# Optimization experiments

Hardware: AMD Instinct MI355X
Metric: run time of the kernel (lower is better)

Reference implementation:

```python
import jax, jax.numpy as jnp
import numpy as np

B, S, IN, OUT = 4, 2048, 4096, 11008


def setup_inputs() -> dict:
    key = jax.random.key(0)
    k1, k2, k3, k4, k5 = jax.random.split(key, 5)
    x = jax.random.normal(k1, (B, S, IN), dtype=jnp.float32)
    # int8 quantized weights, stored as int32 per harness spec but values in int8 range
    W_int8 = jax.random.randint(k2, (OUT, IN), -128, 128, dtype=jnp.int32)
    # per-output-channel scales (small positive) and zero-points
    scale = jax.random.uniform(k3, (OUT,), dtype=jnp.float32, minval=1e-3, maxval=2e-2)
    zero = jax.random.uniform(k4, (OUT,), dtype=jnp.float32, minval=-8.0, maxval=8.0)
    bias = jax.random.normal(k5, (OUT,), dtype=jnp.float32) * 0.01
    return {"x": x, "W_int8": W_int8, "scale": scale, "zero": zero, "bias": bias}


def reference(x, W_int8, scale, zero, bias):
    # Original torch forward raises on NaN/Inf in x; for valid inputs the math is
    # quant_matmul: dequantize W = (W_int8 - zero) * scale (per output channel),
    # then y = x @ W.T + bias.
    W = (W_int8.astype(jnp.float32) - zero[:, None]) * scale[:, None]  # [OUT, IN]
    y = jnp.einsum('bsi,oi->bso', x, W) + bias  # [B, S, OUT]
    return y
```

## Files before the change

### kernel.cpp

```cpp
#include <hip/hip_runtime.h>
#include <stdint.h>


#define M_DIM 8192
#define N_DIM 11008
#define K_DIM 4096
#define NT    (K_DIM / 64)
#define BUFB  24576

typedef __attribute__((ext_vector_type(4))) int i32x4;


__global__ void convert_w_kernel(const int* __restrict__ w,
                                 int8_t* __restrict__ o, int n4) {
  int idx = blockIdx.x * blockDim.x + threadIdx.x;
  int stride = gridDim.x * blockDim.x;
  for (int i = idx; i < n4; i += stride) {
    int4 v = ((const int4*)w)[i];
    int r = (v.x & 255) | ((v.y & 255) << 8) | ((v.z & 255) << 16) | ((v.w & 255) << 24);
    ((int*)o)[i] = r;
  }
}

__global__ __launch_bounds__(256) void quantx_kernel(
    const float* __restrict__ x, int8_t* __restrict__ h8, int8_t* __restrict__ l8,
    float* __restrict__ xs, float* __restrict__ rsum) {
  const int row = blockIdx.x;
  const int t = threadIdx.x;
  const float4* px = (const float4*)(x + (size_t)row * K_DIM);
  float4 v[4];
  float mx = 0.f, sm = 0.f;
  #pragma unroll
  for (int i = 0; i < 4; ++i) {
    v[i] = px[i * 256 + t];
    mx = fmaxf(mx, fmaxf(fmaxf(fabsf(v[i].x), fabsf(v[i].y)),
                         fmaxf(fabsf(v[i].z), fabsf(v[i].w))));
    sm += v[i].x + v[i].y + v[i].z + v[i].w;
  }
  #pragma unroll
  for (int off = 32; off > 0; off >>= 1) {
    mx = fmaxf(mx, __shfl_down(mx, off));
    sm += __shfl_down(sm, off);
  }
  __shared__ float rmx[4], rsm[4];
  const int wv = t >> 6, ln = t & 63;
  if (ln == 0) { rmx[wv] = mx; rsm[wv] = sm; }
  __syncthreads();
  const float rowmax = fmaxf(fmaxf(rmx[0], rmx[1]), fmaxf(rmx[2], rmx[3]));
  if (t == 0) {
    xs[row] = rowmax > 0.f ? rowmax / 16256.f : 0.f;
    rsum[row] = rsm[0] + rsm[1] + rsm[2] + rsm[3];
  }
  const float inv = rowmax > 0.f ? 16256.f / rowmax : 0.f;
  int* hp = (int*)(h8 + (size_t)row * K_DIM);
  int* lp = (int*)(l8 + (size_t)row * K_DIM);
  #pragma unroll
  for (int i = 0; i < 4; ++i) {
    int q0 = (int)rintf(v[i].x * inv);
    int q1 = (int)rintf(v[i].y * inv);
    int q2 = (int)rintf(v[i].z * inv);
    int q3 = (int)rintf(v[i].w * inv);
    int h0 = (q0 + 64) >> 7, h1 = (q1 + 64) >> 7, h2 = (q2 + 64) >> 7, h3 = (q3 + 64) >> 7;
    int l0 = q0 - (h0 << 7), l1 = q1 - (h1 << 7), l2 = q2 - (h2 << 7), l3 = q3 - (h3 << 7);
    hp[i * 256 + t] = (h0 & 255) | ((h1 & 255) << 8) | ((h2 & 255) << 16) | ((h3 & 255) << 24);
    lp[i * 256 + t] = (l0 & 255) | ((l1 & 255) << 8) | ((l2 & 255) << 16) | ((l3 & 255) << 24);
  }
}


__device__ __forceinline__ void stage_tile(
    const int8_t* __restrict__ Ah, const int8_t* __restrict__ Al,
    const int8_t* __restrict__ Bw, size_t a_base, size_t b_base,
    int ks, int srow, int scol, int wave, int8_t* buf) {
  #pragma unroll
  for (int p = 0; p < 2; ++p) {
    const int8_t* g = Ah + a_base + (size_t)(p * 64 + srow) * K_DIM + ks + scol;
    __builtin_amdgcn_global_load_lds((const __attribute__((address_space(1))) void*)g,
        (__attribute__((address_space(3))) void*)(buf + p * 4096 + wave * 1024), 16, 0, 0);
  }
  #pragma unroll
  for (int p = 0; p < 2; ++p) {
    const int8_t* g = Al + a_base + (size_t)(p * 64 + srow) * K_DIM + ks + scol;
    __builtin_amdgcn_global_load_lds((const __attribute__((address_space(1))) void*)g,
        (__attribute__((address_space(3))) void*)(buf + 8192 + p * 4096 + wave * 1024), 16, 0, 0);
  }
  #pragma unroll
  for (int p = 0; p < 2; ++p) {
    const int8_t* g = Bw + b_base + (size_t)(p * 64 + srow) * K_DIM + ks + scol;
    __builtin_amdgcn_global_load_lds((const __attribute__((address_space(1))) void*)g,
        (__attribute__((address_space(3))) void*)(buf + 16384 + p * 4096 + wave * 1024), 16, 0, 0);
  }
}

__global__ __launch_bounds__(256, 2) void qgemm_kernel(
    const int8_t* __restrict__ Ah, const int8_t* __restrict__ Al,
    const int8_t* __restrict__ Bw, const float* __restrict__ xs,
    const float* __restrict__ rowsum, const float* __restrict__ scale,
    const float* __restrict__ zero, const float* __restrict__ bias,
    float* __restrict__ out) {
  __shared__ int8_t smem[2 * BUFB];

  const int tid = threadIdx.x;
  const int wave = tid >> 6;
  const int lane = tid & 63;

  const int bid = blockIdx.x;
  const int wg = (bid & 7) * 688 + (bid >> 3);
  const int group = wg / 688;
  const int rem = wg % 688;
  const int bm = group * 8 + (rem & 7);
  const int bn = rem >> 3;

  const int wr = wave >> 1;
  const int wc = wave & 1;

  i32x4 acch[4][4], accl[4][4];
  #pragma unroll
  for (int i = 0; i < 4; ++i)
    #pragma unroll
    for (int j = 0; j < 4; ++j) {
      acch[i][j] = (i32x4){0, 0, 0, 0};
      accl[i][j] = (i32x4){0, 0, 0, 0};
    }

  const int srow = tid >> 2;
  const int scol = ((((tid & 3) - ((tid >> 3) & 3)) & 3) << 4);
  const size_t a_base = (size_t)(bm * 128) * K_DIM;
  const size_t b_base = (size_t)(bn * 128) * K_DIM;

  const int fr = lane & 15;
  const int g = lane >> 4;
  const int scA = (((g + (fr >> 1)) & 3) << 4);

  int arow[4], brow[4];
  #pragma unroll
  for (int i = 0; i < 4; ++i) {
    arow[i] = (wr * 64 + i * 16 + fr) * 64 + scA;
    brow[i] = (wc * 64 + i * 16 + fr) * 64 + scA;
  }

  stage_tile(Ah, Al, Bw, a_base, b_base, 0, srow, scol, wave, smem);
  asm volatile("s_waitcnt vmcnt(0)" ::: "memory");
  __builtin_amdgcn_s_barrier();

  #pragma unroll 1
  for (int t = 0; t < NT; ++t) {
    const int8_t* buf = smem + (t & 1) * BUFB;
    int8_t* nxt = smem + ((t + 1) & 1) * BUFB;
    const int8_t* ldsAh_ = buf;
    const int8_t* ldsAl_ = buf + 8192;
    const int8_t* ldsB_  = buf + 16384;

    if (t + 1 < NT)
      stage_tile(Ah, Al, Bw, a_base, b_base, (t + 1) * 64, srow, scol, wave, nxt);

    i32x4 af[4][2], bf[4];
    #pragma unroll
    for (int ni = 0; ni < 4; ++ni)
      bf[ni] = *(const i32x4*)(ldsB_ + brow[ni]);
    #pragma unroll
    for (int mi = 0; mi < 4; ++mi) {
      af[mi][0] = *(const i32x4*)(ldsAh_ + arow[mi]);
      af[mi][1] = *(const i32x4*)(ldsAl_ + arow[mi]);
    }

    __builtin_amdgcn_s_setprio(1);
    #pragma unroll
    for (int mi = 0; mi < 4; ++mi)
      #pragma unroll
      for (int ni = 0; ni < 4; ++ni) {
        acch[mi][ni] = __builtin_amdgcn_mfma_i32_16x16x64_i8(af[mi][0], bf[ni], acch[mi][ni], 0, 0, 0);
        accl[mi][ni] = __builtin_amdgcn_mfma_i32_16x16x64_i8(af[mi][1], bf[ni], accl[mi][ni], 0, 0, 0);
      }
    __builtin_amdgcn_s_setprio(0);

    asm volatile("s_waitcnt lgkmcnt(0)" ::: "memory");
    asm volatile("s_waitcnt vmcnt(0)" ::: "memory");
    __builtin_amdgcn_s_barrier();
  }

  const int row0 = bm * 128 + wr * 64;
  const int col0 = bn * 128 + wc * 64;
  float s_[4], sz_[4], b_[4];
  #pragma unroll
  for (int ni = 0; ni < 4; ++ni) {
    const int n = col0 + ni * 16 + fr;
    const float s = scale[n];
    s_[ni] = s;
    sz_[ni] = s * zero[n];
    b_[ni] = bias[n];
  }
  #pragma unroll
  for (int mi = 0; mi < 4; ++mi) {
    #pragma unroll
    for (int j = 0; j < 4; ++j) {
      const int m = row0 + mi * 16 + g * 4 + j;
      const float xsm = xs[m];
      const float rs = rowsum[m];
      float* po = out + (size_t)m * N_DIM + col0;
      #pragma unroll
      for (int ni = 0; ni < 4; ++ni) {
        const float G = xsm * (128.f * (float)acch[mi][ni][j] + (float)accl[mi][ni][j]);
        po[ni * 16 + fr] = s_[ni] * G - sz_[ni] * rs + b_[ni];
      }
    }
  }
}


__global__ void fallback_kernel(const float* __restrict__ x, const int* __restrict__ w,
                                const float* __restrict__ scale, const float* __restrict__ zero,
                                const float* __restrict__ bias, float* __restrict__ out) {
  const int n = blockIdx.x * 16 + (threadIdx.x & 15);
  const int m = blockIdx.y * 16 + (threadIdx.x >> 4);
  const float z = zero[n];
  const float* xr = x + (size_t)m * K_DIM;
  const int* wr = w + (size_t)n * K_DIM;
  float acc = 0.f;
  for (int k = 0; k < K_DIM; ++k) acc += xr[k] * ((float)wr[k] - z);
  out[(size_t)m * N_DIM + n] = scale[n] * acc + bias[n];
}


extern "C" void kernel_launch(void* const* d_in, const int* in_sizes, int n_in,
                              void* d_out, int out_size, void* d_ws, size_t ws_size,
                              hipStream_t stream) {
  const float* x     = (const float*)d_in[0];
  const int*   w     = (const int*)d_in[1];
  const float* scale = (const float*)d_in[2];
  const float* zero  = (const float*)d_in[3];
  const float* bias  = (const float*)d_in[4];
  float* out = (float*)d_out;

  const size_t n_x = (size_t)M_DIM * K_DIM;
  const size_t n_w = (size_t)N_DIM * K_DIM;
  const size_t need = n_x * 2 + n_w + (size_t)M_DIM * 8;

  if (ws_size < need) {
    dim3 gr(N_DIM / 16, M_DIM / 16);
    fallback_kernel<<<gr, 256, 0, stream>>>(x, w, scale, zero, bias, out);
    return;
  }

  int8_t* x_h = (int8_t*)d_ws;
  int8_t* x_l = x_h + n_x;
  int8_t* w_8 = x_l + n_x;
  float* rsum = (float*)(w_8 + n_w);
  float* xs   = rsum + M_DIM;

  convert_w_kernel<<<2048, 256, 0, stream>>>(w, w_8, (int)(n_w / 4));
  quantx_kernel<<<M_DIM, 256, 0, stream>>>(x, x_h, x_l, xs, rsum);

  const int nblocks = (M_DIM / 128) * (N_DIM / 128);
  qgemm_kernel<<<nblocks, 256, 0, stream>>>(x_h, x_l, w_8, xs, rsum,
                                            scale, zero, bias, out);
}
```

Baseline: 824.8 us.

## Widen GEMM tile to 128x256 with 8 waves and 4-stage LDS pipeline

```diff
diff --git a/kernel.cpp b/kernel.cpp
--- a/kernel.cpp
+++ b/kernel.cpp
@@ -5,8 +5,8 @@
 #define M_DIM 8192
 #define N_DIM 11008
 #define K_DIM 4096
-#define NT    (K_DIM / 64)
-#define BUFB  24576
+#define NH    (K_DIM / 64)
+#define BUFH  32768
 
 typedef __attribute__((ext_vector_type(4))) int i32x4;
 
@@ -68,51 +68,87 @@
 }
 
 
-__device__ __forceinline__ void stage_tile(
+__device__ __forceinline__ void stage_half(
     const int8_t* __restrict__ Ah, const int8_t* __restrict__ Al,
     const int8_t* __restrict__ Bw, size_t a_base, size_t b_base,
-    int ks, int srow, int scol, int wave, int8_t* buf) {
+    int h, int trow, int scol, int wave, int8_t* smem) {
+  int8_t* buf = smem + (h & 3) * BUFH;
+  const int ks = h * 64;
+  {
+    const int8_t* g = Ah + a_base + (size_t)trow * K_DIM + ks + scol;
+    __builtin_amdgcn_global_load_lds((const __attribute__((address_space(1))) void*)g,
+        (__attribute__((address_space(3))) void*)(buf + wave * 1024), 16, 0, 0);
+  }
+  {
+    const int8_t* g = Al + a_base + (size_t)trow * K_DIM + ks + scol;
+    __builtin_amdgcn_global_load_lds((const __attribute__((address_space(1))) void*)g,
+        (__attribute__((address_space(3))) void*)(buf + 8192 + wave * 1024), 16, 0, 0);
+  }
   #pragma unroll
   for (int p = 0; p < 2; ++p) {
-    const int8_t* g = Ah + a_base + (size_t)(p * 64 + srow) * K_DIM + ks + scol;
+    const int8_t* g = Bw + b_base + (size_t)(p * 128 + trow) * K_DIM + ks + scol;
     __builtin_amdgcn_global_load_lds((const __attribute__((address_space(1))) void*)g,
-        (__attribute__((address_space(3))) void*)(buf + p * 4096 + wave * 1024), 16, 0, 0);
-  }
-  #pragma unroll
-  for (int p = 0; p < 2; ++p) {
-    const int8_t* g = Al + a_base + (size_t)(p * 64 + srow) * K_DIM + ks + scol;
-    __builtin_amdgcn_global_load_lds((const __attribute__((address_space(1))) void*)g,
-        (__attribute__((address_space(3))) void*)(buf + 8192 + p * 4096 + wave * 1024), 16, 0, 0);
-  }
-  #pragma unroll
-  for (int p = 0; p < 2; ++p) {
-    const int8_t* g = Bw + b_base + (size_t)(p * 64 + srow) * K_DIM + ks + scol;
-    __builtin_amdgcn_global_load_lds((const __attribute__((address_space(1))) void*)g,
-        (__attribute__((address_space(3))) void*)(buf + 16384 + p * 4096 + wave * 1024), 16, 0, 0);
-  }
-}
-
-__global__ __launch_bounds__(256, 2) void qgemm_kernel(
+        (__attribute__((address_space(3))) void*)(buf + 16384 + p * 8192 + wave * 1024), 16, 0, 0);
+  }
+}
+
+__device__ __forceinline__ i32x4 mfma_i8(i32x4 a, i32x4 b, i32x4 c) {
+  return __builtin_amdgcn_mfma_i32_16x16x64_i8(a, b, c, 0, 0, 0);
+}
+
+__device__ __forceinline__ void compute_half(
+    const int8_t* __restrict__ buf, const int* arow, const int* brow,
+    i32x4 (&acch)[4][4], i32x4 (&accl)[4][4]) {
+  const int8_t* pAh = buf;
+  const int8_t* pAl = buf + 8192;
+  const int8_t* pB  = buf + 16384;
+  i32x4 bf[4];
+  #pragma unroll
+  for (int ni = 0; ni < 4; ++ni) bf[ni] = *(const i32x4*)(pB + brow[ni]);
+  i32x4 cah = *(const i32x4*)(pAh + arow[0]);
+  i32x4 cal = *(const i32x4*)(pAl + arow[0]);
+  #pragma unroll
+  for (int mi = 0; mi < 4; ++mi) {
+    i32x4 nah = cah, nal = cal;
+    if (mi < 3) {
+      nah = *(const i32x4*)(pAh + arow[mi + 1]);
+      nal = *(const i32x4*)(pAl + arow[mi + 1]);
+    }
+    __builtin_amdgcn_s_setprio(1);
+    #pragma unroll
+    for (int ni = 0; ni < 4; ++ni)
+      acch[mi][ni] = mfma_i8(cah, bf[ni], acch[mi][ni]);
+    #pragma unroll
+    for (int ni = 0; ni < 4; ++ni)
+      accl[mi][ni] = mfma_i8(cal, bf[ni], accl[mi][ni]);
+    __builtin_amdgcn_s_setprio(0);
+    cah = nah; cal = nal;
+  }
+}
+
+#define VMW(n) asm volatile("s_waitcnt vmcnt(" #n ")" ::: "memory")
+
+__global__ __launch_bounds__(512, 2) void qgemm_kernel(
     const int8_t* __restrict__ Ah, const int8_t* __restrict__ Al,
     const int8_t* __restrict__ Bw, const float* __restrict__ xs,
     const float* __restrict__ rowsum, const float* __restrict__ scale,
     const float* __restrict__ zero, const float* __restrict__ bias,
     float* __restrict__ out) {
-  __shared__ int8_t smem[2 * BUFB];
+  extern __shared__ int8_t smem[];
 
   const int tid = threadIdx.x;
   const int wave = tid >> 6;
   const int lane = tid & 63;
 
   const int bid = blockIdx.x;
-  const int wg = (bid & 7) * 688 + (bid >> 3);
-  const int group = wg / 688;
-  const int rem = wg % 688;
+  const int wg = (bid & 7) * 344 + (bid >> 3);
+  const int group = wg / 344;
+  const int rem = wg % 344;
   const int bm = group * 8 + (rem & 7);
   const int bn = rem >> 3;
 
-  const int wr = wave >> 1;
-  const int wc = wave & 1;
+  const int wr = wave >> 2;
+  const int wc = wave & 3;
 
   i32x4 acch[4][4], accl[4][4];
   #pragma unroll
@@ -123,10 +159,10 @@
       accl[i][j] = (i32x4){0, 0, 0, 0};
     }
 
-  const int srow = tid >> 2;
+  const int trow = tid >> 2;
   const int scol = ((((tid & 3) - ((tid >> 3) & 3)) & 3) << 4);
   const size_t a_base = (size_t)(bm * 128) * K_DIM;
-  const size_t b_base = (size_t)(bn * 128) * K_DIM;
+  const size_t b_base = (size_t)((size_t)bn * 256) * K_DIM;
 
   const int fr = lane & 15;
   const int g = lane >> 4;
@@ -139,48 +175,32 @@
     brow[i] = (wc * 64 + i * 16 + fr) * 64 + scA;
   }
 
-  stage_tile(Ah, Al, Bw, a_base, b_base, 0, srow, scol, wave, smem);
-  asm volatile("s_waitcnt vmcnt(0)" ::: "memory");
-  __builtin_amdgcn_s_barrier();
+  stage_half(Ah, Al, Bw, a_base, b_base, 0, trow, scol, wave, smem);
+  stage_half(Ah, Al, Bw, a_base, b_base, 1, trow, scol, wave, smem);
+  stage_half(Ah, Al, Bw, a_base, b_base, 2, trow, scol, wave, smem);
 
   #pragma unroll 1
-  for (int t = 0; t < NT; ++t) {
-    const int8_t* buf = smem + (t & 1) * BUFB;
-    int8_t* nxt = smem + ((t + 1) & 1) * BUFB;
-    const int8_t* ldsAh_ = buf;
-    const int8_t* ldsAl_ = buf + 8192;
-    const int8_t* ldsB_  = buf + 16384;
-
-    if (t + 1 < NT)
-      stage_tile(Ah, Al, Bw, a_base, b_base, (t + 1) * 64, srow, scol, wave, nxt);
-
-    i32x4 af[4][2], bf[4];
-    #pragma unroll
-    for (int ni = 0; ni < 4; ++ni)
-      bf[ni] = *(const i32x4*)(ldsB_ + brow[ni]);
-    #pragma unroll
-    for (int mi = 0; mi < 4; ++mi) {
-      af[mi][0] = *(const i32x4*)(ldsAh_ + arow[mi]);
-      af[mi][1] = *(const i32x4*)(ldsAl_ + arow[mi]);
-    }
-
-    __builtin_amdgcn_s_setprio(1);
-    #pragma unroll
-    for (int mi = 0; mi < 4; ++mi)
-      #pragma unroll
-      for (int ni = 0; ni < 4; ++ni) {
-        acch[mi][ni] = __builtin_amdgcn_mfma_i32_16x16x64_i8(af[mi][0], bf[ni], acch[mi][ni], 0, 0, 0);
-        accl[mi][ni] = __builtin_amdgcn_mfma_i32_16x16x64_i8(af[mi][1], bf[ni], accl[mi][ni], 0, 0, 0);
-      }
-    __builtin_amdgcn_s_setprio(0);
-
-    asm volatile("s_waitcnt lgkmcnt(0)" ::: "memory");
-    asm volatile("s_waitcnt vmcnt(0)" ::: "memory");
+  for (int h = 0; h < NH - 3; ++h) {
+    stage_half(Ah, Al, Bw, a_base, b_base, h + 3, trow, scol, wave, smem);
+    VMW(12);
     __builtin_amdgcn_s_barrier();
-  }
+    compute_half(smem + (h & 3) * BUFH, arow, brow, acch, accl);
+    __builtin_amdgcn_s_barrier();
+  }
+  VMW(8);
+  __builtin_amdgcn_s_barrier();
+  compute_half(smem + ((NH - 3) & 3) * BUFH, arow, brow, acch, accl);
+  __builtin_amdgcn_s_barrier();
+  VMW(4);
+  __builtin_amdgcn_s_barrier();
+  compute_half(smem + ((NH - 2) & 3) * BUFH, arow, brow, acch, accl);
+  __builtin_amdgcn_s_barrier();
+  VMW(0);
+  __builtin_amdgcn_s_barrier();
+  compute_half(smem + ((NH - 1) & 3) * BUFH, arow, brow, acch, accl);
 
   const int row0 = bm * 128 + wr * 64;
-  const int col0 = bn * 128 + wc * 64;
+  const int col0 = bn * 256 + wc * 64;
   float s_[4], sz_[4], b_[4];
   #pragma unroll
   for (int ni = 0; ni < 4; ++ni) {
@@ -251,7 +271,10 @@
   convert_w_kernel<<<2048, 256, 0, stream>>>(w, w_8, (int)(n_w / 4));
   quantx_kernel<<<M_DIM, 256, 0, stream>>>(x, x_h, x_l, xs, rsum);
 
-  const int nblocks = (M_DIM / 128) * (N_DIM / 128);
-  qgemm_kernel<<<nblocks, 256, 0, stream>>>(x_h, x_l, w_8, xs, rsum,
-                                            scale, zero, bias, out);
-}
+  (void)hipFuncSetAttribute((const void*)qgemm_kernel,
+                            hipFuncAttributeMaxDynamicSharedMemorySize, 4 * BUFH);
+
+  const int nblocks = (M_DIM / 128) * (N_DIM / 256);
+  qgemm_kernel<<<nblocks, 512, 4 * BUFH, stream>>>(x_h, x_l, w_8, xs, rsum,
+                                                   scale, zero, bias, out);
+}
```

New measurement: 805.6 us. 1.02x faster.
